# Kernel tuning notes

Measured on AMD Instinct MI355X. Metric: run time of the kernel, lower is better.

Reference implementation:

```python
import jax, jax.numpy as jnp
import numpy as np

N, E, IN_C, EDGE_D = 100000, 1600000, 16, 4
H1, C1 = 4, 16   # conv1: heads, out channels -> 64
H2, C2 = 4, 16   # conv2: heads, out channels -> 64
G = 64           # num graphs
NUM_MIX, ACTION_DIM, GMM_HID = 3, 10, 64
NEG_SLOPE = 0.2  # PyG GATv2Conv default LeakyReLU slope


def gatv2_layer(x, src, dst, edge_attr, Wl, Wr, We, att, bias, n_nodes, heads, ch):
    # x: [N, Fin] -> out: [N, heads*ch]. Message = alpha * (Wl x)[src];
    # attention logits = att . LeakyReLU((Wl x)[src] + (Wr x)[dst] + We e).
    xl = (x @ Wl).reshape(n_nodes, heads, ch)
    xr = (x @ Wr).reshape(n_nodes, heads, ch)
    ef = (edge_attr @ We).reshape(-1, heads, ch)
    s = jax.nn.leaky_relu(xl[src] + xr[dst] + ef, NEG_SLOPE)      # [E,H,C]
    logits = jnp.einsum('ehc,hc->eh', s, att)                      # [E,H]
    m = jax.ops.segment_max(logits, dst, num_segments=n_nodes)     # [N,H]
    ex = jnp.exp(logits - m[dst])
    denom = jax.ops.segment_sum(ex, dst, num_segments=n_nodes)     # [N,H]
    alpha = ex / denom[dst]                                        # segment softmax over in-edges
    msg = alpha[..., None] * xl[src]                               # [E,H,C]
    out = jax.ops.segment_sum(msg, dst, num_segments=n_nodes)      # [N,H,C]
    return out.reshape(n_nodes, heads * ch) + bias


def global_mean_pool(x, batch, num_graphs):
    s = jax.ops.segment_sum(x, batch, num_segments=num_graphs)
    cnt = jax.ops.segment_sum(jnp.ones((x.shape[0],), x.dtype), batch, num_segments=num_graphs)
    return s / jnp.maximum(cnt, 1.0)[:, None]


def setup_inputs() -> dict:
    key = jax.random.key(0)
    ks = jax.random.split(key, 24)
    sc = 0.1
    x = jax.random.normal(ks[0], (N, IN_C), jnp.float32)
    edge_index = jax.random.randint(ks[1], (2, E), 0, N, jnp.int64)
    edge_attr = jax.random.normal(ks[2], (E, EDGE_D), jnp.float32)
    batch = jnp.sort(jax.random.randint(ks[3], (N,), 0, G, jnp.int64))
    p = {}
    p['Wl1'] = jax.random.normal(ks[4], (IN_C, H1 * C1), jnp.float32) * sc
    p['Wr1'] = jax.random.normal(ks[5], (IN_C, H1 * C1), jnp.float32) * sc
    p['We1'] = jax.random.normal(ks[6], (EDGE_D, H1 * C1), jnp.float32) * sc
    p['att1'] = jax.random.normal(ks[7], (H1, C1), jnp.float32) * sc
    p['b1'] = jnp.zeros((H1 * C1,), jnp.float32)
    p['Wl2'] = jax.random.normal(ks[8], (H1 * C1, H2 * C2), jnp.float32) * sc
    p['Wr2'] = jax.random.normal(ks[9], (H1 * C1, H2 * C2), jnp.float32) * sc
    p['We2'] = jax.random.normal(ks[10], (EDGE_D, H2 * C2), jnp.float32) * sc
    p['att2'] = jax.random.normal(ks[11], (H2, C2), jnp.float32) * sc
    p['b2'] = jnp.zeros((H2 * C2,), jnp.float32)
    p['Wg1'] = jax.random.normal(ks[12], (H2 * C2, GMM_HID), jnp.float32) * sc
    p['bg1'] = jnp.zeros((GMM_HID,), jnp.float32)
    p['Wg2'] = jax.random.normal(ks[13], (GMM_HID, NUM_MIX * 5), jnp.float32) * sc
    p['bg2'] = jnp.zeros((NUM_MIX * 5,), jnp.float32)
    p['Wp'] = jax.random.normal(ks[14], (H2 * C2, ACTION_DIM), jnp.float32) * sc
    p['bp'] = jnp.zeros((ACTION_DIM,), jnp.float32)
    p['Wc1'] = jax.random.normal(ks[15], (H2 * C2, 64), jnp.float32) * sc
    p['bc1'] = jnp.zeros((64,), jnp.float32)
    p['Wc2'] = jax.random.normal(ks[16], (64, 1), jnp.float32) * sc
    p['bc2'] = jnp.zeros((1,), jnp.float32)
    return dict(x=x, edge_index=edge_index, edge_attr=edge_attr, batch=batch, **p)


def reference(x, edge_index, edge_attr, batch,
              Wl1, Wr1, We1, att1, b1,
              Wl2, Wr2, We2, att2, b2,
              Wg1, bg1, Wg2, bg2, Wp, bp, Wc1, bc1, Wc2, bc2):
    src, dst = edge_index[0], edge_index[1]
    y = gatv2_layer(x, src, dst, edge_attr, Wl1, Wr1, We1, att1, b1, N, H1, C1)
    y = jax.nn.elu(y)
    # dropout is identity in eval mode
    y = gatv2_layer(y, src, dst, edge_attr, Wl2, Wr2, We2, att2, b2, N, H2, C2)
    g = global_mean_pool(y, batch, G)                      # [G, H2*C2]
    gmm_params = jax.nn.relu(g @ Wg1 + bg1) @ Wg2 + bg2    # [G, 15]
    num_proposals_logits = g @ Wp + bp                     # [G, 10]
    values = (jax.nn.relu(g @ Wc1 + bc1) @ Wc2 + bc2)[:, 0]  # [G]
    return gmm_params, num_proposals_logits, values
```

## Files before the change

kernel.cpp:

```cpp
#include <hip/hip_runtime.h>

#define DEVINL __device__ __forceinline__

#if __has_builtin(__builtin_amdgcn_exp2f)
DEVINL float fexp2(float x) { return __builtin_amdgcn_exp2f(x); }
#else
DEVINL float fexp2(float x) { return exp2f(x); }
#endif

DEVINL float red4(float pv) {
    pv += __int_as_float(__builtin_amdgcn_ds_swizzle(__float_as_int(pv), 0x041F));
    pv += __int_as_float(__builtin_amdgcn_ds_swizzle(__float_as_int(pv), 0x081F));
    return pv;
}

template <int K>
__global__ void k_lin_tiled(const float* __restrict__ x,
                            const float* __restrict__ Wa,
                            const float* __restrict__ Wb,
                            float* __restrict__ oa, float* __restrict__ ob,
                            int N) {
    __shared__ float sx[64 * K];
    __shared__ float sw[K * 128];
    int t = threadIdx.x;
    int base = blockIdx.x * 64;

    const int WTOT = K * 64 / 4;
    for (int i = t; i < WTOT; i += 256) {
        float4 wa = ((const float4*)Wa)[i];
        float4 wb = ((const float4*)Wb)[i];
        int k = (i * 4) >> 6, f = (i * 4) & 63;
        *(float4*)&sw[k * 128 + f] = wa;
        *(float4*)&sw[k * 128 + 64 + f] = wb;
    }
    const int XTOT = 64 * K / 4;
    for (int i = t; i < XTOT; i += 256) {
        int n = (i * 4) / K, kk = (i * 4) % K;
        float4 v = make_float4(0.f, 0.f, 0.f, 0.f);
        if (base + n < N) v = *(const float4*)&x[(size_t)(base + n) * K + kk];
        *(float4*)&sx[n * K + kk] = v;
    }
    __syncthreads();

    int fq = t & 31;
    int nq = t >> 5;
    float acc[8][4];
#pragma unroll
    for (int i = 0; i < 8; ++i)
#pragma unroll
        for (int c = 0; c < 4; ++c) acc[i][c] = 0.f;

    for (int k0 = 0; k0 < K; k0 += 4) {
        float4 xv[8];
#pragma unroll
        for (int i = 0; i < 8; ++i)
            xv[i] = *(const float4*)&sx[(nq * 8 + i) * K + k0];
#pragma unroll
        for (int kk = 0; kk < 4; ++kk) {
            float4 w = *(const float4*)&sw[(k0 + kk) * 128 + fq * 4];
#pragma unroll
            for (int i = 0; i < 8; ++i) {
                float xs = (kk == 0) ? xv[i].x : (kk == 1) ? xv[i].y
                         : (kk == 2) ? xv[i].z : xv[i].w;
                acc[i][0] = fmaf(xs, w.x, acc[i][0]);
                acc[i][1] = fmaf(xs, w.y, acc[i][1]);
                acc[i][2] = fmaf(xs, w.z, acc[i][2]);
                acc[i][3] = fmaf(xs, w.w, acc[i][3]);
            }
        }
    }

    int col = fq * 4;
    float* o = (col < 64) ? oa : ob;
    int c = col & 63;
#pragma unroll
    for (int i = 0; i < 8; ++i) {
        int n = base + nq * 8 + i;
        if (n < N)
            *(float4*)&o[(size_t)n * 64 + c] =
                make_float4(acc[i][0], acc[i][1], acc[i][2], acc[i][3]);
    }
}

__global__ void k_deg(const int* __restrict__ dst, int* __restrict__ deg, int E) {
    int e = blockIdx.x * blockDim.x + threadIdx.x;
    if (e < E) atomicAdd(&deg[dst[e]], 1);
}

__global__ void k_scan1(const int* __restrict__ deg, int* __restrict__ spart,
                        int* __restrict__ bsum, int N) {
    __shared__ int sh[256];
    int base = blockIdx.x * 1024;
    int t = threadIdx.x;
    int v[4]; int sum = 0;
#pragma unroll
    for (int i = 0; i < 4; ++i) {
        int idx = base + t * 4 + i;
        v[i] = (idx < N) ? deg[idx] : 0;
        sum += v[i];
    }
    sh[t] = sum;
    __syncthreads();
    for (int off = 1; off < 256; off <<= 1) {
        int x = (t >= off) ? sh[t - off] : 0;
        __syncthreads();
        sh[t] += x;
        __syncthreads();
    }
    int run = (t > 0) ? sh[t - 1] : 0;
#pragma unroll
    for (int i = 0; i < 4; ++i) {
        run += v[i];
        int idx = base + t * 4 + i;
        if (idx < N) spart[idx] = run;
    }
    if (t == 255) bsum[blockIdx.x] = sh[255];
}

__global__ void k_scan2(int* __restrict__ bsum, int nb) {
    __shared__ int sh[128];
    int t = threadIdx.x;
    sh[t] = (t < nb) ? bsum[t] : 0;
    __syncthreads();
    for (int off = 1; off < 128; off <<= 1) {
        int x = (t >= off) ? sh[t - off] : 0;
        __syncthreads();
        sh[t] += x;
        __syncthreads();
    }
    if (t < nb) bsum[t] = (t > 0) ? sh[t - 1] : 0;
}

__global__ void k_scan3(const int* __restrict__ spart, const int* __restrict__ bsum,
                        int* __restrict__ rowptr, int N) {
    int i = blockIdx.x * blockDim.x + threadIdx.x;
    if (i < N) rowptr[i + 1] = spart[i] + bsum[i >> 10];
    if (i == 0) rowptr[0] = 0;
}

__global__ void k_binit(const int* __restrict__ rowptr, int* __restrict__ bfill,
                        int shift, int B, int N) {
    int b = blockIdx.x * blockDim.x + threadIdx.x;
    if (b < B) {
        long long node = (long long)b << shift;
        if (node > N) node = N;
        bfill[b] = rowptr[node];
    }
}

__global__ void k_part(const int* __restrict__ src, const int* __restrict__ dst,
                       int* __restrict__ bfill, unsigned long long* __restrict__ stg,
                       int shift, int E, int chunk) {
    __shared__ int hist[512];
    __shared__ int base[512];
    int t = threadIdx.x;
    int e0 = blockIdx.x * chunk;
    int e1 = e0 + chunk; if (e1 > E) e1 = E;
    for (int i = t; i < 512; i += 256) hist[i] = 0;
    __syncthreads();
    for (int e = e0 + t; e < e1; e += 256)
        atomicAdd(&hist[(unsigned)dst[e] >> shift], 1);
    __syncthreads();
    for (int i = t; i < 512; i += 256) {
        int h = hist[i];
        base[i] = h ? atomicAdd(&bfill[i], h) : 0;
    }
    __syncthreads();
    for (int i = t; i < 512; i += 256) hist[i] = 0;
    __syncthreads();
    unsigned mask = (1u << shift) - 1u;
    for (int e = e0 + t; e < e1; e += 256) {
        int d = dst[e];
        int b = (unsigned)d >> shift;
        int off = atomicAdd(&hist[b], 1);
        unsigned long long p = ((unsigned long long)(unsigned)e << 40)
                             | ((unsigned long long)(unsigned)src[e] << 12)
                             | (unsigned long long)((unsigned)d & mask);
        stg[(size_t)(base[b] + off)] = p;
    }
}

__global__ void k_scat2(const unsigned long long* __restrict__ stg,
                        const int* __restrict__ rowptr, int* __restrict__ fill,
                        int2* __restrict__ csr, int shift, int N) {
    int b = blockIdx.x;
    long long n0 = (long long)b << shift; if (n0 > N) n0 = N;
    long long n1 = (long long)(b + 1) << shift; if (n1 > N) n1 = N;
    int s0 = rowptr[n0], s1 = rowptr[n1];
    unsigned mask = (1u << shift) - 1u;
    for (int i = s0 + (int)threadIdx.x; i < s1; i += 256) {
        unsigned long long p = stg[i];
        int dlow = (int)(p & mask);
        int s = (int)((p >> 12) & 0xFFFFFFFu);
        int eid = (int)(p >> 40);
        int d = (b << shift) | dlow;
        int pos = rowptr[d] + atomicAdd(&fill[d], 1);
        csr[pos] = make_int2(s, eid);
    }
}

__global__ void k_scatter(const int* __restrict__ src, const int* __restrict__ dst,
                          const int* __restrict__ rowptr, int* __restrict__ fill,
                          int2* __restrict__ csr, int E) {
    int e = blockIdx.x * blockDim.x + threadIdx.x;
    if (e >= E) return;
    int d = dst[e];
    int pos = rowptr[d] + atomicAdd(&fill[d], 1);
    csr[pos] = make_int2(src[e], e);
}

DEVINL float quad_logit(float4 a, float4 xv, float4 xr4,
                        float4 w0, float4 w1, float4 w2, float4 w3, float4 at) {
    float vx = fmaf(a.x, w0.x, fmaf(a.y, w1.x, fmaf(a.z, w2.x, fmaf(a.w, w3.x, xr4.x)))) + xv.x;
    float vy = fmaf(a.x, w0.y, fmaf(a.y, w1.y, fmaf(a.z, w2.y, fmaf(a.w, w3.y, xr4.y)))) + xv.y;
    float vz = fmaf(a.x, w0.z, fmaf(a.y, w1.z, fmaf(a.z, w2.z, fmaf(a.w, w3.z, xr4.z)))) + xv.z;
    float vw = fmaf(a.x, w0.w, fmaf(a.y, w1.w, fmaf(a.z, w2.w, fmaf(a.w, w3.w, xr4.w)))) + xv.w;
    vx = fmaxf(vx, 0.2f * vx);
    vy = fmaxf(vy, 0.2f * vy);
    vz = fmaxf(vz, 0.2f * vz);
    vw = fmaxf(vw, 0.2f * vw);
    float pv = fmaf(vx, at.x, fmaf(vy, at.y, fmaf(vz, at.z, vw * at.w)));
    return red4(pv);
}

__global__ void k_gat_agg(const int* __restrict__ rowptr,
                          const int2* __restrict__ csr,
                          const float4* __restrict__ ea,
                          const float* __restrict__ xl,
                          const float* __restrict__ xr,
                          const float* __restrict__ We,
                          const float* __restrict__ att,
                          const float* __restrict__ bias,
                          float* __restrict__ out,
                          int N, int elu) {
    int l = threadIdx.x & 63;
    int n = blockIdx.x * 4 + (threadIdx.x >> 6);
    if (n >= N) return;
    int q = l & 15;
    int g = l >> 4;
    int f4 = q * 4;
    const float LOG2E = 1.44269504088896f;

    float4 w0 = *(const float4*)&We[f4];
    float4 w1 = *(const float4*)&We[64 + f4];
    float4 w2 = *(const float4*)&We[128 + f4];
    float4 w3 = *(const float4*)&We[192 + f4];
    float4 at = *(const float4*)&att[f4];
    at.x *= LOG2E; at.y *= LOG2E; at.z *= LOG2E; at.w *= LOG2E;
    float4 xr4 = *(const float4*)&xr[(size_t)n * 64 + f4];

    int beg = rowptr[n], end = rowptr[n + 1];
    const float4* xl4 = (const float4*)xl;

    float m = -1e30f, den = 0.f;
    float4 acc = make_float4(0.f, 0.f, 0.f, 0.f);

    int jb = beg;
    for (; jb + 8 <= end; jb += 8) {
        int2 se0 = csr[jb + g];
        int2 se1 = csr[jb + 4 + g];
        float4 a0 = ea[(unsigned)se0.y];
        float4 a1 = ea[(unsigned)se1.y];
        float4 xv0 = xl4[(unsigned)se0.x * 16u + (unsigned)q];
        float4 xv1 = xl4[(unsigned)se1.x * 16u + (unsigned)q];
        float p0 = quad_logit(a0, xv0, xr4, w0, w1, w2, w3, at);
        float p1 = quad_logit(a1, xv1, xr4, w0, w1, w2, w3, at);
        if (__any(fmaxf(p0, p1) - m > 8.f)) {
            float mn = fmaxf(m, fmaxf(p0, p1));
            float sc = fexp2(m - mn);
            float e0 = fexp2(p0 - mn), e1 = fexp2(p1 - mn);
            den = fmaf(den, sc, e0 + e1);
            acc.x = fmaf(e0, xv0.x, fmaf(e1, xv1.x, acc.x * sc));
            acc.y = fmaf(e0, xv0.y, fmaf(e1, xv1.y, acc.y * sc));
            acc.z = fmaf(e0, xv0.z, fmaf(e1, xv1.z, acc.z * sc));
            acc.w = fmaf(e0, xv0.w, fmaf(e1, xv1.w, acc.w * sc));
            m = mn;
        } else {
            float e0 = fexp2(p0 - m), e1 = fexp2(p1 - m);
            den += e0 + e1;
            acc.x = fmaf(e0, xv0.x, fmaf(e1, xv1.x, acc.x));
            acc.y = fmaf(e0, xv0.y, fmaf(e1, xv1.y, acc.y));
            acc.z = fmaf(e0, xv0.z, fmaf(e1, xv1.z, acc.z));
            acc.w = fmaf(e0, xv0.w, fmaf(e1, xv1.w, acc.w));
        }
    }
    for (; jb < end; jb += 4) {
        int j = jb + g;
        bool valid = (j < end);
        int jj = valid ? j : end - 1;
        int2 se = csr[jj];
        float4 a = ea[(unsigned)se.y];
        float4 xv = xl4[(unsigned)se.x * 16u + (unsigned)q];
        float pv = quad_logit(a, xv, xr4, w0, w1, w2, w3, at);
        pv = valid ? pv : -3.0e38f;
        if (__any(pv - m > 8.f)) {
            float mn = fmaxf(m, pv);
            float sc = fexp2(m - mn);
            float e = fexp2(pv - mn);
            den = fmaf(den, sc, e);
            acc.x = fmaf(e, xv.x, acc.x * sc);
            acc.y = fmaf(e, xv.y, acc.y * sc);
            acc.z = fmaf(e, xv.z, acc.z * sc);
            acc.w = fmaf(e, xv.w, acc.w * sc);
            m = mn;
        } else {
            float e = fexp2(pv - m);
            den += e;
            acc.x = fmaf(e, xv.x, acc.x);
            acc.y = fmaf(e, xv.y, acc.y);
            acc.z = fmaf(e, xv.z, acc.z);
            acc.w = fmaf(e, xv.w, acc.w);
        }
    }

#pragma unroll
    for (int mask = 16; mask <= 32; mask <<= 1) {
        float m2 = __shfl_xor(m, mask);
        float d2 = __shfl_xor(den, mask);
        float ax = __shfl_xor(acc.x, mask);
        float ay = __shfl_xor(acc.y, mask);
        float az = __shfl_xor(acc.z, mask);
        float aw = __shfl_xor(acc.w, mask);
        float mn = fmaxf(m, m2);
        float s1 = fexp2(m - mn);
        float s2 = fexp2(m2 - mn);
        den = den * s1 + d2 * s2;
        acc.x = acc.x * s1 + ax * s2;
        acc.y = acc.y * s1 + ay * s2;
        acc.z = acc.z * s1 + az * s2;
        acc.w = acc.w * s1 + aw * s2;
        m = mn;
    }

    float inv = (den > 0.f) ? 1.f / den : 0.f;
    float4 b4 = *(const float4*)&bias[f4];
    float4 val;
    val.x = fmaf(acc.x, inv, b4.x);
    val.y = fmaf(acc.y, inv, b4.y);
    val.z = fmaf(acc.z, inv, b4.z);
    val.w = fmaf(acc.w, inv, b4.w);
    if (elu) {
        val.x = (val.x > 0.f) ? val.x : expm1f(val.x);
        val.y = (val.y > 0.f) ? val.y : expm1f(val.y);
        val.z = (val.z > 0.f) ? val.z : expm1f(val.z);
        val.w = (val.w > 0.f) ? val.w : expm1f(val.w);
    }
    if (l < 16) ((float4*)out)[(size_t)n * 16 + q] = val;
}

__global__ void k_pool(const float* __restrict__ y2,
                       const int* __restrict__ batch,
                       float* __restrict__ pool, float* __restrict__ cnt, int N) {
    const int CH = 256;
    int f = threadIdx.x & 63;
    int lane = threadIdx.x >> 6;
    int base = blockIdx.x * CH;
    int curg = -1;
    float acc = 0.f;
    float c = 0.f;
    for (int n = base + lane; n < base + CH && n < N; n += 4) {
        int g = batch[n];
        if (g != curg) {
            if (curg >= 0) {
                atomicAdd(pool + (size_t)curg * 64 + f, acc);
                if (f == 0) atomicAdd(cnt + curg, c);
            }
            curg = g; acc = 0.f; c = 0.f;
        }
        acc += y2[(size_t)n * 64 + f];
        c += 1.f;
    }
    if (curg >= 0) {
        atomicAdd(pool + (size_t)curg * 64 + f, acc);
        if (f == 0) atomicAdd(cnt + curg, c);
    }
}

__global__ void k_head(const float* __restrict__ pool, const float* __restrict__ cnt,
                       const float* __restrict__ Wg1, const float* __restrict__ bg1,
                       const float* __restrict__ Wg2, const float* __restrict__ bg2,
                       const float* __restrict__ Wp, const float* __restrict__ bp,
                       const float* __restrict__ Wc1, const float* __restrict__ bc1,
                       const float* __restrict__ Wc2, const float* __restrict__ bc2,
                       float* __restrict__ out) {
    int g = blockIdx.x, f = threadIdx.x;
    __shared__ float sg[64];
    __shared__ float sh[64];
    float inv = 1.f / fmaxf(cnt[g], 1.f);
    sg[f] = pool[(size_t)g * 64 + f] * inv;
    __syncthreads();
    float acc = bg1[f];
    for (int k = 0; k < 64; ++k) acc += sg[k] * Wg1[k * 64 + f];
    sh[f] = fmaxf(acc, 0.f);
    __syncthreads();
    if (f < 15) {
        float o = bg2[f];
        for (int k = 0; k < 64; ++k) o += sh[k] * Wg2[k * 15 + f];
        out[(size_t)g * 15 + f] = o;
    }
    if (f < 10) {
        float o = bp[f];
        for (int k = 0; k < 64; ++k) o += sg[k] * Wp[k * 10 + f];
        out[960 + (size_t)g * 10 + f] = o;
    }
    __syncthreads();
    float acc2 = bc1[f];
    for (int k = 0; k < 64; ++k) acc2 += sg[k] * Wc1[k * 64 + f];
    sh[f] = fmaxf(acc2, 0.f);
    __syncthreads();
    if (f == 0) {
        float v = bc2[0];
        for (int k = 0; k < 64; ++k) v += sh[k] * Wc2[k];
        out[1600 + g] = v;
    }
}

extern "C" void kernel_launch(void* const* d_in, const int* in_sizes, int n_in,
                              void* d_out, int out_size, void* d_ws, size_t ws_size,
                              hipStream_t stream) {
    const float* x     = (const float*)d_in[0];
    const int*   ei    = (const int*)d_in[1];
    const float* ea    = (const float*)d_in[2];
    const int*   batch = (const int*)d_in[3];
    const float* Wl1 = (const float*)d_in[4];
    const float* Wr1 = (const float*)d_in[5];
    const float* We1 = (const float*)d_in[6];
    const float* att1 = (const float*)d_in[7];
    const float* b1  = (const float*)d_in[8];
    const float* Wl2 = (const float*)d_in[9];
    const float* Wr2 = (const float*)d_in[10];
    const float* We2 = (const float*)d_in[11];
    const float* att2 = (const float*)d_in[12];
    const float* b2  = (const float*)d_in[13];
    const float* Wg1 = (const float*)d_in[14];
    const float* bg1 = (const float*)d_in[15];
    const float* Wg2 = (const float*)d_in[16];
    const float* bg2 = (const float*)d_in[17];
    const float* Wp  = (const float*)d_in[18];
    const float* bp  = (const float*)d_in[19];
    const float* Wc1 = (const float*)d_in[20];
    const float* bc1 = (const float*)d_in[21];
    const float* Wc2 = (const float*)d_in[22];
    const float* bc2 = (const float*)d_in[23];

    const int N = in_sizes[0] / 16;
    const int E = in_sizes[2] / 4;
    const int* src = ei;
    const int* dst = ei + E;

    int shift = 8;
    while (((N + (1 << shift) - 1) >> shift) > 512) ++shift;
    int B = (N + (1 << shift) - 1) >> shift;
    bool radix = (shift <= 12) && (N <= (1 << 28)) && (E < (1 << 24));

    size_t NF = (size_t)N * 64;
    char* w = (char*)d_ws;
    float* A  = (float*)w; w += NF * 4;
    float* B_ = (float*)w; w += NF * 4;
    float* C  = (float*)w; w += NF * 4;
    int2* csr = (int2*)w;  w += (size_t)E * 8;
    int* rowptr = (int*)w; w += (size_t)(N + 1) * 4;
    int* deg    = (int*)w; w += (size_t)N * 4;
    int* spart  = (int*)w; w += (size_t)N * 4;
    int* bsum   = (int*)w; w += 128 * 4;
    int* bfill  = (int*)w; w += 513 * 4;
    float* PL   = (float*)w; w += 4096 * 4;
    float* CT   = (float*)w;
    unsigned long long* stg = (unsigned long long*)A;
    radix = radix && ((size_t)E * 8 <= NF * 4);

    dim3 blk(256);
    int gE  = (E + 255) / 256;
    int gN  = (N + 255) / 256;
    int nb1 = (N + 1023) / 1024;
    int gAgg = (N + 3) / 4;
    int gLin = (N + 63) / 64;

    hipMemsetAsync(deg, 0, (size_t)N * sizeof(int), stream);
    k_deg<<<gE, blk, 0, stream>>>(dst, deg, E);
    k_scan1<<<nb1, blk, 0, stream>>>(deg, spart, bsum, N);
    k_scan2<<<1, 128, 0, stream>>>(bsum, nb1);
    k_scan3<<<gN, blk, 0, stream>>>(spart, bsum, rowptr, N);
    hipMemsetAsync(deg, 0, (size_t)N * sizeof(int), stream);
    if (radix) {
        k_binit<<<(B + 255) / 256, blk, 0, stream>>>(rowptr, bfill, shift, B, N);
        int gridA = 512;
        int chunk = (E + gridA - 1) / gridA;
        k_part<<<gridA, blk, 0, stream>>>(src, dst, bfill, stg, shift, E, chunk);
        k_scat2<<<B, blk, 0, stream>>>(stg, rowptr, deg, csr, shift, N);
    } else {
        k_scatter<<<gE, blk, 0, stream>>>(src, dst, rowptr, deg, csr, E);
    }

    k_lin_tiled<16><<<gLin, blk, 0, stream>>>(x, Wl1, Wr1, A, B_, N);
    k_gat_agg<<<gAgg, blk, 0, stream>>>(rowptr, csr, (const float4*)ea, A, B_,
                                        We1, att1, b1, C, N, 1);

    k_lin_tiled<64><<<gLin, blk, 0, stream>>>(C, Wl2, Wr2, B_, A, N);
    k_gat_agg<<<gAgg, blk, 0, stream>>>(rowptr, csr, (const float4*)ea, B_, A,
                                        We2, att2, b2, C, N, 0);

    hipMemsetAsync(PL, 0, (4096 + 64) * sizeof(float), stream);
    k_pool<<<(N + 255) / 256, blk, 0, stream>>>(C, batch, PL, CT, N);
    k_head<<<64, 64, 0, stream>>>(PL, CT, Wg1, bg1, Wg2, bg2, Wp, bp,
                                  Wc1, bc1, Wc2, bc2, (float*)d_out);
}
```

Before: 460.9 us.

## Fuse scatter with first linear layer and fold fill reset and bucket init into scan

The layer-1 linear transform now runs as extra blocks of the CSR scatter kernel, so the two independent jobs share one launch and can overlap. The fill-counter memset and the bucket-offset init kernel are folded into the final scan kernel, which computes bucket offsets directly from the partial sums. The staging buffer moves from A to C so the fused linear kernel can write A without clobbering staged edges. Together these remove two launches and a memset, at the cost of a larger combined grid and mixed block roles that share shared-memory sizing.

```diff
diff --git a/kernel.cpp b/kernel.cpp
--- a/kernel.cpp
+++ b/kernel.cpp
@@ -15,16 +15,12 @@
 }
 
 template <int K>
-__global__ void k_lin_tiled(const float* __restrict__ x,
-                            const float* __restrict__ Wa,
-                            const float* __restrict__ Wb,
-                            float* __restrict__ oa, float* __restrict__ ob,
-                            int N) {
-    __shared__ float sx[64 * K];
-    __shared__ float sw[K * 128];
-    int t = threadIdx.x;
-    int base = blockIdx.x * 64;
-
+DEVINL void lin_body(float* sx, float* sw,
+                     const float* __restrict__ x,
+                     const float* __restrict__ Wa,
+                     const float* __restrict__ Wb,
+                     float* __restrict__ oa, float* __restrict__ ob,
+                     int N, int base, int t) {
     const int WTOT = K * 64 / 4;
     for (int i = t; i < WTOT; i += 256) {
         float4 wa = ((const float4*)Wa)[i];
@@ -82,6 +78,17 @@
     }
 }
 
+template <int K>
+__global__ void k_lin_tiled(const float* __restrict__ x,
+                            const float* __restrict__ Wa,
+                            const float* __restrict__ Wb,
+                            float* __restrict__ oa, float* __restrict__ ob,
+                            int N) {
+    __shared__ float sx[64 * K];
+    __shared__ float sw[K * 128];
+    lin_body<K>(sx, sw, x, Wa, Wb, oa, ob, N, blockIdx.x * 64, threadIdx.x);
+}
+
 __global__ void k_deg(const int* __restrict__ dst, int* __restrict__ deg, int E) {
     int e = blockIdx.x * blockDim.x + threadIdx.x;
     if (e < E) atomicAdd(&deg[dst[e]], 1);
@@ -132,19 +139,19 @@
 }
 
 __global__ void k_scan3(const int* __restrict__ spart, const int* __restrict__ bsum,
-                        int* __restrict__ rowptr, int N) {
+                        int* __restrict__ rowptr, int* __restrict__ fill,
+                        int* __restrict__ bfill, int shift, int B, int N) {
     int i = blockIdx.x * blockDim.x + threadIdx.x;
-    if (i < N) rowptr[i + 1] = spart[i] + bsum[i >> 10];
+    if (i < N) {
+        rowptr[i + 1] = spart[i] + bsum[i >> 10];
+        fill[i] = 0;
+    }
     if (i == 0) rowptr[0] = 0;
-}
-
-__global__ void k_binit(const int* __restrict__ rowptr, int* __restrict__ bfill,
-                        int shift, int B, int N) {
-    int b = blockIdx.x * blockDim.x + threadIdx.x;
-    if (b < B) {
-        long long node = (long long)b << shift;
+    if (i < B) {
+        long long node = (long long)i << shift;
         if (node > N) node = N;
-        bfill[b] = rowptr[node];
+        bfill[i] = (node == 0) ? 0
+                 : spart[node - 1] + bsum[(int)((node - 1) >> 10)];
     }
 }
 
@@ -180,22 +187,33 @@
     }
 }
 
-__global__ void k_scat2(const unsigned long long* __restrict__ stg,
-                        const int* __restrict__ rowptr, int* __restrict__ fill,
-                        int2* __restrict__ csr, int shift, int N) {
-    int b = blockIdx.x;
-    long long n0 = (long long)b << shift; if (n0 > N) n0 = N;
-    long long n1 = (long long)(b + 1) << shift; if (n1 > N) n1 = N;
-    int s0 = rowptr[n0], s1 = rowptr[n1];
-    unsigned mask = (1u << shift) - 1u;
-    for (int i = s0 + (int)threadIdx.x; i < s1; i += 256) {
-        unsigned long long p = stg[i];
-        int dlow = (int)(p & mask);
-        int s = (int)((p >> 12) & 0xFFFFFFFu);
-        int eid = (int)(p >> 40);
-        int d = (b << shift) | dlow;
-        int pos = rowptr[d] + atomicAdd(&fill[d], 1);
-        csr[pos] = make_int2(s, eid);
+__global__ void k_scat2_lin1(const unsigned long long* __restrict__ stg,
+                             const int* __restrict__ rowptr, int* __restrict__ fill,
+                             int2* __restrict__ csr, int shift, int N, int B,
+                             const float* __restrict__ x,
+                             const float* __restrict__ Wa,
+                             const float* __restrict__ Wb,
+                             float* __restrict__ oa, float* __restrict__ ob) {
+    __shared__ float sx[64 * 16];
+    __shared__ float sw[16 * 128];
+    if ((int)blockIdx.x < B) {
+        int b = blockIdx.x;
+        long long n0 = (long long)b << shift; if (n0 > N) n0 = N;
+        long long n1 = (long long)(b + 1) << shift; if (n1 > N) n1 = N;
+        int s0 = rowptr[n0], s1 = rowptr[n1];
+        unsigned mask = (1u << shift) - 1u;
+        for (int i = s0 + (int)threadIdx.x; i < s1; i += 256) {
+            unsigned long long p = stg[i];
+            int dlow = (int)(p & mask);
+            int s = (int)((p >> 12) & 0xFFFFFFFu);
+            int eid = (int)(p >> 40);
+            int d = (b << shift) | dlow;
+            int pos = rowptr[d] + atomicAdd(&fill[d], 1);
+            csr[pos] = make_int2(s, eid);
+        }
+    } else {
+        lin_body<16>(sx, sw, x, Wa, Wb, oa, ob, N,
+                     ((int)blockIdx.x - B) * 64, threadIdx.x);
     }
 }
 
@@ -466,7 +484,7 @@
     int* bfill  = (int*)w; w += 513 * 4;
     float* PL   = (float*)w; w += 4096 * 4;
     float* CT   = (float*)w;
-    unsigned long long* stg = (unsigned long long*)A;
+    unsigned long long* stg = (unsigned long long*)C;
     radix = radix && ((size_t)E * 8 <= NF * 4);
 
     dim3 blk(256);
@@ -480,19 +498,18 @@
     k_deg<<<gE, blk, 0, stream>>>(dst, deg, E);
     k_scan1<<<nb1, blk, 0, stream>>>(deg, spart, bsum, N);
     k_scan2<<<1, 128, 0, stream>>>(bsum, nb1);
-    k_scan3<<<gN, blk, 0, stream>>>(spart, bsum, rowptr, N);
-    hipMemsetAsync(deg, 0, (size_t)N * sizeof(int), stream);
+    k_scan3<<<gN, blk, 0, stream>>>(spart, bsum, rowptr, deg, bfill, shift, B, N);
     if (radix) {
-        k_binit<<<(B + 255) / 256, blk, 0, stream>>>(rowptr, bfill, shift, B, N);
         int gridA = 512;
         int chunk = (E + gridA - 1) / gridA;
         k_part<<<gridA, blk, 0, stream>>>(src, dst, bfill, stg, shift, E, chunk);
-        k_scat2<<<B, blk, 0, stream>>>(stg, rowptr, deg, csr, shift, N);
+        k_scat2_lin1<<<B + gLin, blk, 0, stream>>>(stg, rowptr, deg, csr, shift,
+                                                   N, B, x, Wl1, Wr1, A, B_);
     } else {
         k_scatter<<<gE, blk, 0, stream>>>(src, dst, rowptr, deg, csr, E);
-    }
-
-    k_lin_tiled<16><<<gLin, blk, 0, stream>>>(x, Wl1, Wr1, A, B_, N);
+        k_lin_tiled<16><<<gLin, blk, 0, stream>>>(x, Wl1, Wr1, A, B_, N);
+    }
+
     k_gat_agg<<<gAgg, blk, 0, stream>>>(rowptr, csr, (const float4*)ea, A, B_,
                                         We1, att1, b1, C, N, 1);
 
```

Result: no change. 453.3 us (-1.7%).
